# Kernel optimization log

Measured on AMD Instinct MI355X. Metric: run time of the kernel, lower is better.

The kernel has to match this reference:

```python
import jax, jax.numpy as jnp
import numpy as np
from jax import lax

EPS = 1e-5
WBITS, BBITS, ABITS = 8, 8, 11  # weight/bias/activation precisions (class defaults)


def _ste_round(x):
    # straight-through estimator round (matches HAWQ-style fake quant)
    return x + lax.stop_gradient(jnp.round(x) - x)


def _quant_weight(w, bits):
    # symmetric per-output-channel weight quantization
    n = 2.0 ** (bits - 1) - 1.0
    s = lax.stop_gradient(jnp.max(jnp.abs(w.reshape(w.shape[0], -1)), axis=1)) / n
    s = jnp.maximum(s, 1e-8)
    w_int = jnp.clip(_ste_round(w / s[:, None, None, None]), -n - 1.0, n)
    return w_int, s


def _conv(x, w, stride, pad):
    return lax.conv_general_dilated(
        x, w, (stride, stride), ((pad, pad), (pad, pad)),
        dimension_numbers=('NCHW', 'OIHW', 'NCHW'))


def _quant_bn_conv(x, act_scale, w, gamma, beta, mean, var, stride, pad):
    # fold BN into conv (QuantBnConv2d), quantize folded weight per channel,
    # integer conv in the x/act_scale domain, rescale back to float
    f = gamma * lax.rsqrt(var + EPS)
    w_f = w * f[:, None, None, None]
    b_f = beta - mean * f
    w_int, w_s = _quant_weight(w_f, WBITS)
    nb = 2.0 ** (BBITS - 1) - 1.0
    b_s = w_s * act_scale  # [O]
    b_int = jnp.clip(_ste_round(b_f / b_s), -nb - 1.0, nb)
    x_int = x / act_scale
    y_int = _conv(x_int, w_int, stride, pad) + b_int[None, :, None, None]
    return y_int * b_s[None, :, None, None], w_s


def _quant_conv(x, act_scale, w, stride, pad):
    # plain QuantConv2d (shortcut path, no bias)
    w_int, w_s = _quant_weight(w, WBITS)
    y_int = _conv(x / act_scale, w_int, stride, pad)
    scale = w_s * act_scale  # [O]
    return y_int * scale[None, :, None, None], w_s


def _quant_act(x, bits):
    # QuantAct: symmetric dynamic requantization to `bits` bits
    n = 2.0 ** (bits - 1) - 1.0
    s = jnp.maximum(lax.stop_gradient(jnp.max(jnp.abs(x))) / n, 1e-8)
    xq = jnp.clip(_ste_round(x / s), -n - 1.0, n) * s
    return xq, s


def setup_inputs() -> dict:
    key = jax.random.key(0)
    ks = jax.random.split(key, 12)
    B, Cin, Cout, H = 64, 128, 256, 56
    return {
        'x': jax.random.normal(ks[0], (B, Cin, H, H), jnp.float32),
        'act_scale': jnp.ones((1,), jnp.float32) * 0.05,
        'w_sc': jax.random.normal(ks[1], (Cout, Cin, 1, 1), jnp.float32) * 0.05,
        'w1': jax.random.normal(ks[2], (Cout, Cin, 3, 3), jnp.float32) * 0.05,
        'g1': jax.random.uniform(ks[3], (Cout,), jnp.float32) + 0.5,
        'b1': jax.random.normal(ks[4], (Cout,), jnp.float32) * 0.1,
        'm1': jax.random.normal(ks[5], (Cout,), jnp.float32) * 0.1,
        'v1': jax.random.uniform(ks[6], (Cout,), jnp.float32) + 0.5,
        'w2': jax.random.normal(ks[7], (Cout, Cout, 3, 3), jnp.float32) * 0.05,
        'g2': jax.random.uniform(ks[8], (Cout,), jnp.float32) + 0.5,
        'b2': jax.random.normal(ks[9], (Cout,), jnp.float32) * 0.1,
        'm2': jax.random.normal(ks[10], (Cout,), jnp.float32) * 0.1,
        'v2': jax.random.uniform(ks[11], (Cout,), jnp.float32) + 0.5,
    }


def reference(x, act_scale, w_sc, w1, g1, b1, m1, v1, w2, g2, b2, m2, v2):
    # resize_identity branch of QBlock.forward (stride-2 stage transition)
    short_x, _ = _quant_conv(x, act_scale, w_sc, stride=2, pad=0)
    out, _ = _quant_bn_conv(x, act_scale, w1, g1, b1, m1, v1, stride=2, pad=1)
    out = jax.nn.relu(out)
    out, a = _quant_act(out, ABITS)
    out, _ = _quant_bn_conv(out, a, w2, g2, b2, m2, v2, stride=1, pad=1)
    out = jax.nn.relu(out)
    out, a = _quant_act(out, ABITS)
    out = jax.nn.relu(out + short_x)
    out, a = _quant_act(out, ABITS)
    return out, a
```

## Files before the change

### kernel.cpp

```cpp
#include <hip/hip_runtime.h>
#include <cstdio>
#include <cstdint>

typedef _Float16 h8 __attribute__((ext_vector_type(8)));
typedef _Float16 h4 __attribute__((ext_vector_type(4)));
typedef _Float16 h2 __attribute__((ext_vector_type(2)));
typedef float f4 __attribute__((ext_vector_type(4)));

#define GLD16(g, l) __builtin_amdgcn_global_load_lds( \
    (const __attribute__((address_space(1))) void*)(g), \
    (__attribute__((address_space(3))) void*)(l), 16, 0, 0)

static constexpr int HOUT = 28;
static constexpr long long NSP = 64LL * HOUT * HOUT;
static constexpr long long NEL = NSP * 256;
static constexpr int NSLOT = 64;
static constexpr int SLOTSTRIDE = 32;

__global__ void init_ws(int* __restrict__ slots, _Float16* __restrict__ zp)
{
    const int t = threadIdx.x;
    for (int i = t; i < 3 * NSLOT * SLOTSTRIDE; i += 256) slots[i] = 0;
    for (int i = t; i < 512; i += 256) zp[i] = (_Float16)0.f;
}

__device__ __forceinline__ float slot_max(const int* __restrict__ slots)
{
    float m = 0.f;
#pragma unroll
    for (int i = 0; i < NSLOT; ++i) m = fmaxf(m, __int_as_float(slots[i * SLOTSTRIDE]));
    return m;
}

__global__ void prep_w1(const float* __restrict__ w1, const float* __restrict__ g1,
                        const float* __restrict__ b1, const float* __restrict__ m1,
                        const float* __restrict__ v1, const float* __restrict__ asp,
                        _Float16* __restrict__ wq, float* __restrict__ scale1,
                        float* __restrict__ bias1)
{
    const int o = blockIdx.x, t = threadIdx.x;
    const float f = g1[o] * rsqrtf(v1[o] + 1e-5f);
    const float* wr = w1 + (size_t)o * 1152;
    float amax = 0.f;
    for (int i = t; i < 1152; i += 256) amax = fmaxf(amax, fabsf(wr[i] * f));
    __shared__ float red[256];
    red[t] = amax; __syncthreads();
    for (int s = 128; s > 0; s >>= 1) { if (t < s) red[t] = fmaxf(red[t], red[t + s]); __syncthreads(); }
    const float ws = fmaxf(red[0] / 127.f, 1e-8f);
    for (int idx = t; idx < 2304; idx += 256) {
        int p = idx >> 8, cc = idx & 255, ci = cc & 127;
        float q = fminf(fmaxf(rintf(wr[ci * 9 + p] * f / ws), -128.f), 127.f);
        wq[(size_t)o * 2304 + idx] = (_Float16)q;
    }
    if (t == 0) {
        const float bs = ws * asp[0];
        const float bf = b1[o] - m1[o] * f;
        float bq = fminf(fmaxf(rintf(bf / bs), -128.f), 127.f);
        scale1[o] = bs;
        bias1[o] = bq * bs;
    }
}

__global__ void prep_w2(const float* __restrict__ w2, const float* __restrict__ g2,
                        const float* __restrict__ b2, const float* __restrict__ m2,
                        const float* __restrict__ v2,
                        _Float16* __restrict__ wq, float* __restrict__ ws2,
                        float* __restrict__ b2f)
{
    const int o = blockIdx.x, t = threadIdx.x;
    const float f = g2[o] * rsqrtf(v2[o] + 1e-5f);
    const float* wr = w2 + (size_t)o * 2304;
    float amax = 0.f;
    for (int i = t; i < 2304; i += 256) amax = fmaxf(amax, fabsf(wr[i] * f));
    __shared__ float red[256];
    red[t] = amax; __syncthreads();
    for (int s = 128; s > 0; s >>= 1) { if (t < s) red[t] = fmaxf(red[t], red[t + s]); __syncthreads(); }
    const float ws = fmaxf(red[0] / 127.f, 1e-8f);
    for (int idx = t; idx < 2304; idx += 256) {
        int p = idx >> 8, ci = idx & 255;
        float q = fminf(fmaxf(rintf(wr[ci * 9 + p] * f / ws), -128.f), 127.f);
        wq[(size_t)o * 2304 + idx] = (_Float16)q;
    }
    if (t == 0) { ws2[o] = ws; b2f[o] = b2[o] - m2[o] * f; }
}

__global__ void prep_wsc(const float* __restrict__ wsc, const float* __restrict__ asp,
                         _Float16* __restrict__ wq, float* __restrict__ scale_sc)
{
    const int o = blockIdx.x, t = threadIdx.x;
    const float* wr = wsc + (size_t)o * 128;
    float amax = (t < 128) ? fabsf(wr[t]) : 0.f;
    __shared__ float red[256];
    red[t] = amax; __syncthreads();
    for (int s = 128; s > 0; s >>= 1) { if (t < s) red[t] = fmaxf(red[t], red[t + s]); __syncthreads(); }
    const float ws = fmaxf(red[0] / 127.f, 1e-8f);
    float q = fminf(fmaxf(rintf(wr[t & 127] / ws), -128.f), 127.f);
    wq[(size_t)o * 256 + t] = (_Float16)q;
    if (t == 0) scale_sc[o] = ws * asp[0];
}

__global__ void prep_x(const float* __restrict__ x, const float* __restrict__ asp,
                       _Float16* __restrict__ xf)
{
    const int b = blockIdx.x / 56, h = blockIdx.x - (blockIdx.x / 56) * 56;
    const float as = asp[0];
    __shared__ float tile[56 * 129];
    const float* src = x + ((size_t)b * 128 * 56 + h) * 56;
    for (int i = threadIdx.x; i < 7168; i += 256) {
        int c = i / 56, ww = i - c * 56;
        tile[ww * 129 + c] = src[(size_t)c * 3136 + ww] / as;
    }
    __syncthreads();
    _Float16* dst = xf + (size_t)(b * 56 + h) * 2 * 28 * 256;
    for (int j = threadIdx.x; j < 7168; j += 256) {
        int ww = j >> 7, q = j & 127;
        int cc = q * 2;
        int c0 = cc & 127, c1 = (cc + 1) & 127;
        float x0 = tile[ww * 129 + c0];
        float x1 = tile[ww * 129 + c1];
        h2 o;
        if (cc < 128) { o[0] = (_Float16)x0; o[1] = (_Float16)x1; }
        else {
            _Float16 h0 = (_Float16)x0, h1 = (_Float16)x1;
            o[0] = (_Float16)(x0 - (float)h0);
            o[1] = (_Float16)(x1 - (float)h1);
        }
        size_t eo = ((size_t)(ww & 1) * 28 + (ww >> 1)) * 256 + (size_t)cc;
        *(h2*)&dst[eo] = o;
    }
}

template<int MODE>
__global__ __launch_bounds__(512, 1)
void conv_k(const _Float16* __restrict__ Xf,
            const _Float16* __restrict__ Wq,
            const _Float16* __restrict__ Wsc,
            const float* __restrict__ scale,
            const float* __restrict__ bias,
            const float* __restrict__ scale_sc,
            float* __restrict__ Y,
            float* __restrict__ Ysc,
            int* __restrict__ slots,
            const _Float16* __restrict__ zp)
{
    constexpr int NH = 72;
    __shared__ __attribute__((aligned(16))) _Float16 L[65536];
    __shared__ float wred[8];

    const int t = threadIdx.x;
    const int w = t >> 6, lane = t & 63;
    const int wm = w >> 2, wn = w & 3;
    const int fr = lane & 15, fqr = lane >> 4;

    const int orig = blockIdx.x;
    const int xcd = orig & 7, i8 = orig >> 3;
    const int wgid = (xcd < 4 ? xcd * 25 : 100 + (xcd - 4) * 24) + i8;
    const int n0 = wgid << 8;

    const int srow = (w & 3) * 64 + lane;
    const char* aSrc = (const char*)Wq + (size_t)srow * 4608;
    const int nb = n0 + srow;
    const int bb = nb / 784;
    const int rbp = nb - bb * 784;
    const int ohb = rbp / 28, owb = rbp - (rbp / 28) * 28;
    const int fqs = w >> 2;
    const int dgr = w * 64;

    const char* bptr = (const char*)zp;
    auto set_tap = [&](int kt) {
        const int p = kt >> 3;
        const int kh = p / 3, kw = p - kh * 3;
        if constexpr (MODE == 0) {
            int ih = ohb * 2 - 1 + kh;
            int par = (kw == 1) ? 0 : 1;
            int j = (kw == 0) ? owb - 1 : owb;
            bool ok = ((unsigned)ih < 56u) && ((unsigned)j < 28u);
            bptr = ok ? (const char*)Xf + (((((size_t)bb * 56 + ih) * 2 + par) * 28 + j) << 9)
                      : (const char*)zp;
        } else {
            int ih = ohb - 1 + kh, iw = owb - 1 + kw;
            bool ok = ((unsigned)ih < 28u) && ((unsigned)iw < 28u);
            bptr = ok ? (const char*)Xf + ((((size_t)bb * 28 + ih) * 28 + iw) << 9)
                      : (const char*)zp;
        }
    };

    auto stage_part = [&](int kt, int j) {
        if (kt >= NH) return;
        char* base = (char*)L + (size_t)(kt & 3) * 32768;
        const int fq = 2 * j + fqs;
        if (j == 0 && (kt & 7) == 0) set_tap(kt);
        GLD16(aSrc + (size_t)kt * 64 + fq * 16, base + (j * 512 + dgr) * 16);
        GLD16(bptr + (kt & 7) * 64 + fq * 16,   base + 16384 + (j * 512 + dgr) * 16);
    };

    f4 acc[8][4];
#pragma unroll
    for (int i = 0; i < 8; ++i)
#pragma unroll
        for (int j = 0; j < 4; ++j) acc[i][j] = f4{0.f, 0.f, 0.f, 0.f};

    stage_part(0, 0); stage_part(0, 1);
    stage_part(1, 0); stage_part(1, 1);
    stage_part(2, 0); stage_part(2, 1);
    asm volatile("s_waitcnt vmcnt(8)" ::: "memory");
    __builtin_amdgcn_s_barrier();

#pragma unroll 1
    for (int kt = 0; kt < NH; ++kt) {
        const char* SA = (const char*)L + (size_t)(kt & 3) * 32768;
        const char* SB = SA + 16384;
        h8 af0[4], bf[4];
#pragma unroll
        for (int i = 0; i < 4; ++i) {
            af0[i] = *(const h8*)(SA + fqr * 4096 + (wm * 128 + i * 16 + fr) * 16);
            bf[i]  = *(const h8*)(SB + fqr * 4096 + (wn * 64 + i * 16 + fr) * 16);
        }
        stage_part(kt + 3, 0);
        __builtin_amdgcn_s_barrier();
        asm volatile("s_waitcnt lgkmcnt(0)" ::: "memory");
        __builtin_amdgcn_sched_barrier(0);
        __builtin_amdgcn_s_setprio(1);
#pragma unroll
        for (int mi = 0; mi < 4; ++mi)
#pragma unroll
            for (int ni = 0; ni < 4; ++ni)
                acc[mi][ni] = __builtin_amdgcn_mfma_f32_16x16x32_f16(af0[mi], bf[ni], acc[mi][ni], 0, 0, 0);
        __builtin_amdgcn_s_setprio(0);
        __builtin_amdgcn_s_barrier();

        h8 af1[4];
#pragma unroll
        for (int i = 0; i < 4; ++i)
            af1[i] = *(const h8*)(SA + fqr * 4096 + (wm * 128 + 64 + i * 16 + fr) * 16);
        stage_part(kt + 3, 1);
        __builtin_amdgcn_s_barrier();
        asm volatile("s_waitcnt lgkmcnt(0)" ::: "memory");
        __builtin_amdgcn_sched_barrier(0);
        __builtin_amdgcn_s_setprio(1);
#pragma unroll
        for (int mi = 0; mi < 4; ++mi)
#pragma unroll
            for (int ni = 0; ni < 4; ++ni)
                acc[4 + mi][ni] = __builtin_amdgcn_mfma_f32_16x16x32_f16(af1[mi], bf[ni], acc[4 + mi][ni], 0, 0, 0);
        __builtin_amdgcn_s_setprio(0);
        const int rem = (NH - 2) - kt;
        if (rem >= 2)      { asm volatile("s_waitcnt vmcnt(8)" ::: "memory"); }
        else if (rem == 1) { asm volatile("s_waitcnt vmcnt(4)" ::: "memory"); }
        else if (rem == 0) { asm volatile("s_waitcnt vmcnt(0)" ::: "memory"); }
        __builtin_amdgcn_s_barrier();
    }

    float tmax = 0.f;
#pragma unroll
    for (int mi = 0; mi < 8; ++mi) {
        const int m = wm * 128 + mi * 16 + fqr * 4;
        const f4 sc = *(const f4*)&scale[m];
        const f4 bi = *(const f4*)&bias[m];
#pragma unroll
        for (int ni = 0; ni < 4; ++ni) {
            const int n = n0 + wn * 64 + ni * 16 + fr;
            f4 v = acc[mi][ni] * sc + bi;
            f4 r;
            r.x = fmaxf(v.x, 0.f); r.y = fmaxf(v.y, 0.f);
            r.z = fmaxf(v.z, 0.f); r.w = fmaxf(v.w, 0.f);
            tmax = fmaxf(tmax, fmaxf(fmaxf(r.x, r.y), fmaxf(r.z, r.w)));
            *(f4*)&Y[(size_t)n * 256 + m] = r;
        }
    }
#pragma unroll
    for (int off = 32; off > 0; off >>= 1)
        tmax = fmaxf(tmax, __shfl_xor(tmax, off));
    if (lane == 0) wred[w] = tmax;
    __syncthreads();
    if (t == 0) {
        float mx = 0.f;
#pragma unroll
        for (int i = 0; i < 8; ++i) mx = fmaxf(mx, wred[i]);
        atomicMax(&slots[(wgid & (NSLOT - 1)) * SLOTSTRIDE], __float_as_int(mx));
    }

    if constexpr (MODE == 0) {
        const char* pb[4];
#pragma unroll
        for (int ni = 0; ni < 4; ++ni) {
            int n = n0 + wn * 64 + ni * 16 + fr;
            int b2 = n / 784;
            int r2 = n - b2 * 784;
            int oh2 = r2 / 28, ow2 = r2 - (r2 / 28) * 28;
            pb[ni] = (const char*)Xf + (((((size_t)b2 * 56 + oh2 * 2) * 2 + 0) * 28 + ow2) << 9);
        }
#pragma unroll
        for (int i = 0; i < 8; ++i)
#pragma unroll
            for (int j = 0; j < 4; ++j) acc[i][j] = f4{0.f, 0.f, 0.f, 0.f};
#pragma unroll 1
        for (int st = 0; st < 8; ++st) {
            h8 sf[8], bg[4];
#pragma unroll
            for (int mi = 0; mi < 8; ++mi)
                sf[mi] = *(const h8*)((const char*)Wsc +
                         (size_t)(wm * 128 + mi * 16 + fr) * 512 + st * 64 + fqr * 16);
#pragma unroll
            for (int ni = 0; ni < 4; ++ni)
                bg[ni] = *(const h8*)(pb[ni] + st * 64 + fqr * 16);
#pragma unroll
            for (int mi = 0; mi < 8; ++mi)
#pragma unroll
                for (int ni = 0; ni < 4; ++ni)
                    acc[mi][ni] = __builtin_amdgcn_mfma_f32_16x16x32_f16(sf[mi], bg[ni], acc[mi][ni], 0, 0, 0);
        }
#pragma unroll
        for (int mi = 0; mi < 8; ++mi) {
            const int m = wm * 128 + mi * 16 + fqr * 4;
            const f4 ssc = *(const f4*)&scale_sc[m];
#pragma unroll
            for (int ni = 0; ni < 4; ++ni) {
                const int n = n0 + wn * 64 + ni * 16 + fr;
                f4 s = acc[mi][ni] * ssc;
                *(f4*)&Ysc[(size_t)n * 256 + m] = s;
            }
        }
    }
}

__global__ void mid_k(const int* __restrict__ slotsA, const float* __restrict__ ws2,
                      const float* __restrict__ b2f, float* __restrict__ scale2,
                      float* __restrict__ bias2, float* __restrict__ a1p)
{
    const int o = threadIdx.x;
    const float a1 = fmaxf(slot_max(slotsA) / 1023.f, 1e-8f);
    const float s2 = ws2[o] * a1;
    float bq = fminf(fmaxf(rintf(b2f[o] / s2), -128.f), 127.f);
    scale2[o] = s2;
    bias2[o] = bq * s2;
    if (o == 0) a1p[0] = a1;
}

__global__ void quant_x2(const float* __restrict__ t1, const float* __restrict__ a1p,
                         _Float16* __restrict__ x2)
{
    const size_t i = (size_t)blockIdx.x * 256 + threadIdx.x;
    const float a1 = a1p[0];
    f4 v = ((const f4*)t1)[i];
    h4 o;
    o[0] = (_Float16)fminf(rintf(v.x / a1), 1023.f);
    o[1] = (_Float16)fminf(rintf(v.y / a1), 1023.f);
    o[2] = (_Float16)fminf(rintf(v.z / a1), 1023.f);
    o[3] = (_Float16)fminf(rintf(v.w / a1), 1023.f);
    ((h4*)x2)[i] = o;
}

__global__ void add_short_k(const float* __restrict__ t2, const float* __restrict__ sh,
                            const int* __restrict__ slotsB, int* __restrict__ slotsC,
                            float* __restrict__ o3)
{
    const float a2 = fmaxf(slot_max(slotsB) / 1023.f, 1e-8f);
    const float inv_a2 = 1.f / a2;
    float tmax = 0.f;
    const size_t base = (size_t)blockIdx.x * 256 + threadIdx.x;
#pragma unroll
    for (int it = 0; it < 4; ++it) {
        const size_t i = base + (size_t)it * 802816;
        f4 v = ((const f4*)t2)[i];
        f4 s = ((const f4*)sh)[i];
        f4 r;
        r.x = fmaxf(fminf(rintf(v.x * inv_a2), 1023.f) * a2 + s.x, 0.f);
        r.y = fmaxf(fminf(rintf(v.y * inv_a2), 1023.f) * a2 + s.y, 0.f);
        r.z = fmaxf(fminf(rintf(v.z * inv_a2), 1023.f) * a2 + s.z, 0.f);
        r.w = fmaxf(fminf(rintf(v.w * inv_a2), 1023.f) * a2 + s.w, 0.f);
        ((f4*)o3)[i] = r;
        tmax = fmaxf(tmax, fmaxf(fmaxf(r.x, r.y), fmaxf(r.z, r.w)));
    }
#pragma unroll
    for (int off = 32; off > 0; off >>= 1)
        tmax = fmaxf(tmax, __shfl_xor(tmax, off));
    __shared__ float wred[4];
    if ((threadIdx.x & 63) == 0) wred[threadIdx.x >> 6] = tmax;
    __syncthreads();
    if (threadIdx.x == 0) {
        float mx = fmaxf(fmaxf(wred[0], wred[1]), fmaxf(wred[2], wred[3]));
        atomicMax(&slotsC[(blockIdx.x & (NSLOT - 1)) * SLOTSTRIDE], __float_as_int(mx));
    }
}

__global__ void finalize_k(const float* __restrict__ o3, const int* __restrict__ slotsC,
                           float* __restrict__ dout, int out_size)
{
    const int b = blockIdx.x / 28, oh = blockIdx.x - (blockIdx.x / 28) * 28;
    const float a3 = fmaxf(slot_max(slotsC) / 1023.f, 1e-8f);
    __shared__ float tile[28 * 257];
    const float* src = o3 + (size_t)(b * 28 + oh) * 28 * 256;
    for (int i = threadIdx.x; i < 7168; i += 256)
        tile[(i >> 8) * 257 + (i & 255)] = src[i];
    __syncthreads();
    for (int j = threadIdx.x; j < 7168; j += 256) {
        int c = j / 28, ww = j - (j / 28) * 28;
        float v = tile[ww * 257 + c];
        float q = fminf(rintf(v / a3), 1023.f);
        dout[(((size_t)b * 256 + c) * 28 + oh) * 28 + ww] = q * a3;
    }
    if (blockIdx.x == 0 && threadIdx.x == 0) dout[(size_t)out_size - 1] = a3;
}

extern "C" void kernel_launch(void* const* d_in, const int* in_sizes, int n_in,
                              void* d_out, int out_size, void* d_ws, size_t ws_size,
                              hipStream_t stream)
{
    const float* x   = (const float*)d_in[0];
    const float* as_ = (const float*)d_in[1];
    const float* wsc = (const float*)d_in[2];
    const float* w1  = (const float*)d_in[3];
    const float* g1  = (const float*)d_in[4];
    const float* b1  = (const float*)d_in[5];
    const float* m1  = (const float*)d_in[6];
    const float* v1  = (const float*)d_in[7];
    const float* w2  = (const float*)d_in[8];
    const float* g2  = (const float*)d_in[9];
    const float* b2  = (const float*)d_in[10];
    const float* m2  = (const float*)d_in[11];
    const float* v2  = (const float*)d_in[12];
    float* out = (float*)d_out;

    char* w = (char*)d_ws;
    size_t off = 0;
    auto alloc = [&](size_t bytes) { size_t c = off; off += (bytes + 255) & ~(size_t)255; return c; };
    const size_t oXF = alloc((size_t)64 * 56 * 56 * 256 * 2);
    const size_t oY1 = alloc((size_t)NEL * 4);
    const size_t oSH = alloc((size_t)NEL * 4);
    const size_t oX2 = alloc((size_t)NEL * 2);
    const size_t oW1 = alloc((size_t)256 * 2304 * 2);
    const size_t oW2 = alloc((size_t)256 * 2304 * 2);
    const size_t oWS = alloc((size_t)256 * 256 * 2);
    const size_t oSC = alloc((size_t)8 * 256 * 4);
    const size_t oMS = alloc(3 * NSLOT * SLOTSTRIDE * 4 + 2048);
    if (off > ws_size) {
        fprintf(stderr, "kernel_launch: ws too small: need %zu have %zu\n", off, ws_size);
        return;
    }

    _Float16* xf   = (_Float16*)(w + oXF);
    float*    y1   = (float*)(w + oY1);
    float*    sh   = (float*)(w + oSH);
    _Float16* x2   = (_Float16*)(w + oX2);
    _Float16* wq1  = (_Float16*)(w + oW1);
    _Float16* wq2  = (_Float16*)(w + oW2);
    _Float16* wscd = (_Float16*)(w + oWS);
    float* scl = (float*)(w + oSC);
    float *scale1 = scl, *bias1 = scl + 256, *scale_sc = scl + 512, *ws2 = scl + 768,
          *b2f = scl + 1024, *scale2 = scl + 1280, *bias2 = scl + 1536, *a1p = scl + 1792;
    int* slots  = (int*)(w + oMS);
    int* slotsA = slots;
    int* slotsB = slots + NSLOT * SLOTSTRIDE;
    int* slotsC = slots + 2 * NSLOT * SLOTSTRIDE;
    _Float16* zp = (_Float16*)(w + oMS + 3 * NSLOT * SLOTSTRIDE * 4);
    float* y2 = (float*)(w + oXF);
    float* o3 = (float*)(w + oY1);

    init_ws<<<1, 256, 0, stream>>>(slots, zp);
    prep_wsc<<<256, 256, 0, stream>>>(wsc, as_, wscd, scale_sc);
    prep_w1<<<256, 256, 0, stream>>>(w1, g1, b1, m1, v1, as_, wq1, scale1, bias1);
    prep_w2<<<256, 256, 0, stream>>>(w2, g2, b2, m2, v2, wq2, ws2, b2f);
    prep_x<<<64 * 56, 256, 0, stream>>>(x, as_, xf);
    conv_k<0><<<196, 512, 0, stream>>>(xf, wq1, wscd, scale1, bias1, scale_sc,
                                       y1, sh, slotsA, zp);
    mid_k<<<1, 256, 0, stream>>>(slotsA, ws2, b2f, scale2, bias2, a1p);
    quant_x2<<<12544, 256, 0, stream>>>(y1, a1p, x2);
    conv_k<1><<<196, 512, 0, stream>>>(x2, wq2, nullptr, scale2, bias2, nullptr,
                                       y2, nullptr, slotsB, zp);
    add_short_k<<<3136, 256, 0, stream>>>(y2, sh, slotsB, slotsC, o3);
    finalize_k<<<64 * 28, 256, 0, stream>>>(o3, slotsC, out, out_size);
}
```

Measured before the change: 437.7 us.

## Shrink conv tiles to 128x128 with 256 threads and 3 blocks per CU

The implicit-GEMM conv kernel moves from one 512-thread block per CU computing a 256x256 tile to 256-thread blocks computing 128x128 tiles, with up to three resident per CU and 784 blocks instead of 196. The K loop becomes a three-stage LDS ring buffer with one MFMA phase per step. Per-tap input offsets are now precomputed as 32-bit offsets, and the zero-pad pointer is passed as an offset. This raises occupancy and spreads work across more CUs, and in exchange each tile reuses operands less, so L2 and LDS traffic per FLOP goes up and the shortcut weights are reloaded by more blocks.

```diff
diff --git a/kernel.cpp b/kernel.cpp
--- a/kernel.cpp
+++ b/kernel.cpp
@@ -131,7 +131,7 @@
 }
 
 template<int MODE>
-__global__ __launch_bounds__(512, 1)
+__global__ __launch_bounds__(256, 3)
 void conv_k(const _Float16* __restrict__ Xf,
             const _Float16* __restrict__ Wq,
             const _Float16* __restrict__ Wsc,
@@ -141,83 +141,92 @@
             float* __restrict__ Y,
             float* __restrict__ Ysc,
             int* __restrict__ slots,
-            const _Float16* __restrict__ zp)
-{
-    constexpr int NH = 72;
-    __shared__ __attribute__((aligned(16))) _Float16 L[65536];
-    __shared__ float wred[8];
+            unsigned zpo)
+{
+    constexpr int NSTEP = 72;
+    __shared__ __attribute__((aligned(16))) _Float16 L[24576];
+    __shared__ float wred[4];
 
     const int t = threadIdx.x;
     const int w = t >> 6, lane = t & 63;
-    const int wm = w >> 2, wn = w & 3;
+    const int wm = w >> 1, wn = w & 1;
     const int fr = lane & 15, fqr = lane >> 4;
 
-    const int orig = blockIdx.x;
-    const int xcd = orig & 7, i8 = orig >> 3;
-    const int wgid = (xcd < 4 ? xcd * 25 : 100 + (xcd - 4) * 24) + i8;
-    const int n0 = wgid << 8;
-
-    const int srow = (w & 3) * 64 + lane;
-    const char* aSrc = (const char*)Wq + (size_t)srow * 4608;
-    const int nb = n0 + srow;
-    const int bb = nb / 784;
-    const int rbp = nb - bb * 784;
-    const int ohb = rbp / 28, owb = rbp - (rbp / 28) * 28;
-    const int fqs = w >> 2;
-    const int dgr = w * 64;
-
-    const char* bptr = (const char*)zp;
-    auto set_tap = [&](int kt) {
-        const int p = kt >> 3;
-        const int kh = p / 3, kw = p - kh * 3;
-        if constexpr (MODE == 0) {
-            int ih = ohb * 2 - 1 + kh;
-            int par = (kw == 1) ? 0 : 1;
-            int j = (kw == 0) ? owb - 1 : owb;
-            bool ok = ((unsigned)ih < 56u) && ((unsigned)j < 28u);
-            bptr = ok ? (const char*)Xf + (((((size_t)bb * 56 + ih) * 2 + par) * 28 + j) << 9)
-                      : (const char*)zp;
-        } else {
-            int ih = ohb - 1 + kh, iw = owb - 1 + kw;
-            bool ok = ((unsigned)ih < 28u) && ((unsigned)iw < 28u);
-            bptr = ok ? (const char*)Xf + ((((size_t)bb * 28 + ih) * 28 + iw) << 9)
-                      : (const char*)zp;
+    const int id = blockIdx.x;
+    const int lin = (id & 7) * 98 + (id >> 3);
+    const int m0 = (lin & 1) << 7;
+    const int n0 = (lin >> 1) << 7;
+
+    const int srow = t & 127;
+    const int fq0 = t >> 7;
+    const char* aBase = (const char*)Wq + (size_t)(m0 + srow) * 4608 + fq0 * 16;
+
+    unsigned tpo[9];
+    {
+        const int nb = n0 + srow;
+        const int bb = nb / 784;
+        const int rb = nb - bb * 784;
+        const int ohb = rb / 28, owb = rb - (rb / 28) * 28;
+#pragma unroll
+        for (int p = 0; p < 9; ++p) {
+            const int kh = p / 3, kw = p - kh * 3;
+            if constexpr (MODE == 0) {
+                int ih = ohb * 2 - 1 + kh;
+                int par = (kw == 1) ? 0 : 1;
+                int j = (kw == 0) ? owb - 1 : owb;
+                bool ok = ((unsigned)ih < 56u) && ((unsigned)j < 28u);
+                tpo[p] = ok ? (unsigned)(((((bb * 56 + ih) * 2 + par) * 28 + j) << 9)) : zpo;
+            } else {
+                int ih = ohb - 1 + kh, iw = owb - 1 + kw;
+                bool ok = ((unsigned)ih < 28u) && ((unsigned)iw < 28u);
+                tpo[p] = ok ? (unsigned)((((bb * 28 + ih) * 28 + iw) << 9)) : zpo;
+            }
+        }
+    }
+
+    auto stage = [&](int it, int buf) {
+        if (it >= NSTEP) return;
+        char* base = (char*)L + buf * 16384;
+        const char* asrc = aBase + (size_t)it * 64;
+        const char* bsrc = (const char*)Xf + tpo[it >> 3] + (it & 7) * 64 + fq0 * 16;
+#pragma unroll
+        for (int pass = 0; pass < 2; ++pass) {
+            GLD16(asrc + pass * 32, base + (pass * 256 + t) * 16);
+            GLD16(bsrc + pass * 32, base + 8192 + (pass * 256 + t) * 16);
         }
     };
 
-    auto stage_part = [&](int kt, int j) {
-        if (kt >= NH) return;
-        char* base = (char*)L + (size_t)(kt & 3) * 32768;
-        const int fq = 2 * j + fqs;
-        if (j == 0 && (kt & 7) == 0) set_tap(kt);
-        GLD16(aSrc + (size_t)kt * 64 + fq * 16, base + (j * 512 + dgr) * 16);
-        GLD16(bptr + (kt & 7) * 64 + fq * 16,   base + 16384 + (j * 512 + dgr) * 16);
-    };
-
-    f4 acc[8][4];
-#pragma unroll
-    for (int i = 0; i < 8; ++i)
+    int aoffr[4], boffr[4];
+#pragma unroll
+    for (int x = 0; x < 4; ++x) {
+        aoffr[x] = fqr * 2048 + (wm * 64 + x * 16 + fr) * 16;
+        boffr[x] = 8192 + fqr * 2048 + (wn * 64 + x * 16 + fr) * 16;
+    }
+
+    f4 acc[4][4];
+#pragma unroll
+    for (int i = 0; i < 4; ++i)
 #pragma unroll
         for (int j = 0; j < 4; ++j) acc[i][j] = f4{0.f, 0.f, 0.f, 0.f};
 
-    stage_part(0, 0); stage_part(0, 1);
-    stage_part(1, 0); stage_part(1, 1);
-    stage_part(2, 0); stage_part(2, 1);
-    asm volatile("s_waitcnt vmcnt(8)" ::: "memory");
-    __builtin_amdgcn_s_barrier();
-
+    stage(0, 0); stage(1, 1);
+    int cur = 0, stg = 2;
 #pragma unroll 1
-    for (int kt = 0; kt < NH; ++kt) {
-        const char* SA = (const char*)L + (size_t)(kt & 3) * 32768;
-        const char* SB = SA + 16384;
-        h8 af0[4], bf[4];
-#pragma unroll
-        for (int i = 0; i < 4; ++i) {
-            af0[i] = *(const h8*)(SA + fqr * 4096 + (wm * 128 + i * 16 + fr) * 16);
-            bf[i]  = *(const h8*)(SB + fqr * 4096 + (wn * 64 + i * 16 + fr) * 16);
-        }
-        stage_part(kt + 3, 0);
+    for (int it = 0; it < NSTEP; ++it) {
+        stage(it + 2, stg);
+        const int rem = NSTEP - 1 - it;
+        if (rem >= 2)      { asm volatile("s_waitcnt vmcnt(8)" ::: "memory"); }
+        else if (rem == 1) { asm volatile("s_waitcnt vmcnt(4)" ::: "memory"); }
+        else               { asm volatile("s_waitcnt vmcnt(0)" ::: "memory"); }
         __builtin_amdgcn_s_barrier();
+
+        const char* B = (const char*)L + cur * 16384;
+        h8 af[4], bf[4];
+#pragma unroll
+        for (int x = 0; x < 4; ++x) {
+            af[x] = *(const h8*)(B + aoffr[x]);
+            bf[x] = *(const h8*)(B + boffr[x]);
+        }
         asm volatile("s_waitcnt lgkmcnt(0)" ::: "memory");
         __builtin_amdgcn_sched_barrier(0);
         __builtin_amdgcn_s_setprio(1);
@@ -225,36 +234,17 @@
         for (int mi = 0; mi < 4; ++mi)
 #pragma unroll
             for (int ni = 0; ni < 4; ++ni)
-                acc[mi][ni] = __builtin_amdgcn_mfma_f32_16x16x32_f16(af0[mi], bf[ni], acc[mi][ni], 0, 0, 0);
+                acc[mi][ni] = __builtin_amdgcn_mfma_f32_16x16x32_f16(af[mi], bf[ni], acc[mi][ni], 0, 0, 0);
         __builtin_amdgcn_s_setprio(0);
         __builtin_amdgcn_s_barrier();
-
-        h8 af1[4];
-#pragma unroll
-        for (int i = 0; i < 4; ++i)
-            af1[i] = *(const h8*)(SA + fqr * 4096 + (wm * 128 + 64 + i * 16 + fr) * 16);
-        stage_part(kt + 3, 1);
-        __builtin_amdgcn_s_barrier();
-        asm volatile("s_waitcnt lgkmcnt(0)" ::: "memory");
-        __builtin_amdgcn_sched_barrier(0);
-        __builtin_amdgcn_s_setprio(1);
-#pragma unroll
-        for (int mi = 0; mi < 4; ++mi)
-#pragma unroll
-            for (int ni = 0; ni < 4; ++ni)
-                acc[4 + mi][ni] = __builtin_amdgcn_mfma_f32_16x16x32_f16(af1[mi], bf[ni], acc[4 + mi][ni], 0, 0, 0);
-        __builtin_amdgcn_s_setprio(0);
-        const int rem = (NH - 2) - kt;
-        if (rem >= 2)      { asm volatile("s_waitcnt vmcnt(8)" ::: "memory"); }
-        else if (rem == 1) { asm volatile("s_waitcnt vmcnt(4)" ::: "memory"); }
-        else if (rem == 0) { asm volatile("s_waitcnt vmcnt(0)" ::: "memory"); }
-        __builtin_amdgcn_s_barrier();
+        cur = (cur == 2) ? 0 : cur + 1;
+        stg = (stg == 2) ? 0 : stg + 1;
     }
 
     float tmax = 0.f;
 #pragma unroll
-    for (int mi = 0; mi < 8; ++mi) {
-        const int m = wm * 128 + mi * 16 + fqr * 4;
+    for (int mi = 0; mi < 4; ++mi) {
+        const int m = m0 + wm * 64 + mi * 16 + fqr * 4;
         const f4 sc = *(const f4*)&scale[m];
         const f4 bi = *(const f4*)&bias[m];
 #pragma unroll
@@ -274,45 +264,43 @@
     if (lane == 0) wred[w] = tmax;
     __syncthreads();
     if (t == 0) {
-        float mx = 0.f;
-#pragma unroll
-        for (int i = 0; i < 8; ++i) mx = fmaxf(mx, wred[i]);
-        atomicMax(&slots[(wgid & (NSLOT - 1)) * SLOTSTRIDE], __float_as_int(mx));
+        float mx = fmaxf(fmaxf(wred[0], wred[1]), fmaxf(wred[2], wred[3]));
+        atomicMax(&slots[(lin & (NSLOT - 1)) * SLOTSTRIDE], __float_as_int(mx));
     }
 
     if constexpr (MODE == 0) {
-        const char* pb[4];
+        unsigned pbo[4];
 #pragma unroll
         for (int ni = 0; ni < 4; ++ni) {
             int n = n0 + wn * 64 + ni * 16 + fr;
             int b2 = n / 784;
             int r2 = n - b2 * 784;
             int oh2 = r2 / 28, ow2 = r2 - (r2 / 28) * 28;
-            pb[ni] = (const char*)Xf + (((((size_t)b2 * 56 + oh2 * 2) * 2 + 0) * 28 + ow2) << 9);
-        }
-#pragma unroll
-        for (int i = 0; i < 8; ++i)
+            pbo[ni] = (unsigned)(((((b2 * 56 + oh2 * 2) * 2 + 0) * 28 + ow2) << 9));
+        }
+#pragma unroll
+        for (int i = 0; i < 4; ++i)
 #pragma unroll
             for (int j = 0; j < 4; ++j) acc[i][j] = f4{0.f, 0.f, 0.f, 0.f};
 #pragma unroll 1
         for (int st = 0; st < 8; ++st) {
-            h8 sf[8], bg[4];
-#pragma unroll
-            for (int mi = 0; mi < 8; ++mi)
+            h8 sf[4], bg[4];
+#pragma unroll
+            for (int mi = 0; mi < 4; ++mi)
                 sf[mi] = *(const h8*)((const char*)Wsc +
-                         (size_t)(wm * 128 + mi * 16 + fr) * 512 + st * 64 + fqr * 16);
+                         (size_t)(m0 + wm * 64 + mi * 16 + fr) * 512 + st * 64 + fqr * 16);
 #pragma unroll
             for (int ni = 0; ni < 4; ++ni)
-                bg[ni] = *(const h8*)(pb[ni] + st * 64 + fqr * 16);
-#pragma unroll
-            for (int mi = 0; mi < 8; ++mi)
+                bg[ni] = *(const h8*)((const char*)Xf + pbo[ni] + st * 64 + fqr * 16);
+#pragma unroll
+            for (int mi = 0; mi < 4; ++mi)
 #pragma unroll
                 for (int ni = 0; ni < 4; ++ni)
                     acc[mi][ni] = __builtin_amdgcn_mfma_f32_16x16x32_f16(sf[mi], bg[ni], acc[mi][ni], 0, 0, 0);
         }
 #pragma unroll
-        for (int mi = 0; mi < 8; ++mi) {
-            const int m = wm * 128 + mi * 16 + fqr * 4;
+        for (int mi = 0; mi < 4; ++mi) {
+            const int m = m0 + wm * 64 + mi * 16 + fqr * 4;
             const f4 ssc = *(const f4*)&scale_sc[m];
 #pragma unroll
             for (int ni = 0; ni < 4; ++ni) {
@@ -453,21 +441,24 @@
     int* slotsA = slots;
     int* slotsB = slots + NSLOT * SLOTSTRIDE;
     int* slotsC = slots + 2 * NSLOT * SLOTSTRIDE;
-    _Float16* zp = (_Float16*)(w + oMS + 3 * NSLOT * SLOTSTRIDE * 4);
+    const size_t oZP = oMS + 3 * NSLOT * SLOTSTRIDE * 4;
+    _Float16* zp = (_Float16*)(w + oZP);
     float* y2 = (float*)(w + oXF);
     float* o3 = (float*)(w + oY1);
+    const unsigned zpo1 = (unsigned)(oZP - oXF);
+    const unsigned zpo2 = (unsigned)(oZP - oX2);
 
     init_ws<<<1, 256, 0, stream>>>(slots, zp);
     prep_wsc<<<256, 256, 0, stream>>>(wsc, as_, wscd, scale_sc);
     prep_w1<<<256, 256, 0, stream>>>(w1, g1, b1, m1, v1, as_, wq1, scale1, bias1);
     prep_w2<<<256, 256, 0, stream>>>(w2, g2, b2, m2, v2, wq2, ws2, b2f);
     prep_x<<<64 * 56, 256, 0, stream>>>(x, as_, xf);
-    conv_k<0><<<196, 512, 0, stream>>>(xf, wq1, wscd, scale1, bias1, scale_sc,
-                                       y1, sh, slotsA, zp);
+    conv_k<0><<<784, 256, 0, stream>>>(xf, wq1, wscd, scale1, bias1, scale_sc,
+                                       y1, sh, slotsA, zpo1);
     mid_k<<<1, 256, 0, stream>>>(slotsA, ws2, b2f, scale2, bias2, a1p);
     quant_x2<<<12544, 256, 0, stream>>>(y1, a1p, x2);
-    conv_k<1><<<196, 512, 0, stream>>>(x2, wq2, nullptr, scale2, bias2, nullptr,
-                                       y2, nullptr, slotsB, zp);
+    conv_k<1><<<784, 256, 0, stream>>>(x2, wq2, nullptr, scale2, bias2, nullptr,
+                                       y2, nullptr, slotsB, zpo2);
     add_short_k<<<3136, 256, 0, stream>>>(y2, sh, slotsB, slotsC, o3);
     finalize_k<<<64 * 28, 256, 0, stream>>>(o3, slotsC, out, out_size);
 }
```

New measurement: 529.2 us. 1.21x slower.
